# Optimization experiments

Hardware: AMD Instinct MI355X
Metric: run time of the kernel (lower is better)

Reference implementation:

```python
import math
import jax, jax.numpy as jnp
import numpy as np
from jax import lax

# FPN anchor layout: 1024x768 image, strides {4,8,16,32,64}, 3 anchors/location
NUM_PER_LEVEL = (147456, 36864, 9216, 2304, 576)
A_TOTAL = sum(NUM_PER_LEVEL)
BATCH = 8
PRE_NMS_TOP_N = 1000   # testing
POST_NMS_TOP_N = 1000  # testing
NMS_THRESH = 0.7
SCORE_THRESH = 0.0
MIN_SIZE = 1.0
IMG_H, IMG_W = 768.0, 1024.0
BBOX_XFORM_CLIP = math.log(1000.0 / 16.0)


def setup_inputs() -> dict:
    key = jax.random.key(0)
    k1, k2, k3, k4, k5, k6 = jax.random.split(key, 6)
    objectness = jax.random.normal(k1, (BATCH, A_TOTAL), jnp.float32)
    pred_bbox_deltas = jax.random.normal(k2, (BATCH, A_TOTAL, 4), jnp.float32) * 0.2
    # valid anchor boxes (x1, y1, x2, y2)
    cx = jax.random.uniform(k3, (A_TOTAL,), jnp.float32) * IMG_W
    cy = jax.random.uniform(k4, (A_TOTAL,), jnp.float32) * IMG_H
    w = 16.0 + jax.random.uniform(k5, (A_TOTAL,), jnp.float32) * 176.0
    h = 16.0 + jax.random.uniform(k6, (A_TOTAL,), jnp.float32) * 176.0
    anchors = jnp.stack([cx - 0.5 * w, cy - 0.5 * h, cx + 0.5 * w, cy + 0.5 * h], -1)
    return {"objectness": objectness, "pred_bbox_deltas": pred_bbox_deltas, "anchors": anchors}


def _nms_image(boxes, scores, lvl, valid):
    """batched_nms (level-offset trick) + post-NMS top-k, fixed shapes.
    boxes [K,4], scores [K], lvl [K] int, valid [K] bool -> [POST_NMS_TOP_N, 5]"""
    K = boxes.shape[0]
    s = jnp.where(valid, scores, -1.0)
    order = jnp.argsort(-s)  # decreasing score (invalid last)
    b = boxes[order]
    s = s[order]
    v = valid[order]
    # offset boxes per level so cross-level boxes never overlap (torchvision batched_nms)
    offset = lvl[order].astype(b.dtype) * (jnp.max(lax.stop_gradient(boxes)) + 1.0)
    nb = lax.stop_gradient(b) + offset[:, None]
    area = (nb[:, 2] - nb[:, 0]) * (nb[:, 3] - nb[:, 1])
    lt = jnp.maximum(nb[:, None, :2], nb[None, :, :2])  # [K,K,2]
    rb = jnp.minimum(nb[:, None, 2:], nb[None, :, 2:])
    wh = jnp.clip(rb - lt, 0.0)
    inter = wh[..., 0] * wh[..., 1]
    iou = inter / jnp.maximum(area[:, None] + area[None, :] - inter, 1e-9)
    pos = jnp.arange(K)

    def body(keep, i):
        sup = keep[i] & (iou[i] > NMS_THRESH) & (pos > i)
        return keep & ~sup, None

    keep, _ = lax.scan(body, v, pos)
    masked = jnp.where(keep, s, -1.0)
    top_s, top_i = lax.top_k(masked, POST_NMS_TOP_N)  # kept, decreasing score
    sel_b = b[top_i]
    ok = top_s > -0.5
    sel_b = jnp.where(ok[:, None], sel_b, 0.0)
    top_s = jnp.where(ok, top_s, 0.0)
    return jnp.concatenate([sel_b, top_s[:, None]], axis=-1)


def reference(objectness, pred_bbox_deltas, anchors):
    # --- box decode (BoxCoder, weights (1,1,1,1)) ---
    wa = anchors[:, 2] - anchors[:, 0]
    ha = anchors[:, 3] - anchors[:, 1]
    cxa = anchors[:, 0] + 0.5 * wa
    cya = anchors[:, 1] + 0.5 * ha
    dx, dy = pred_bbox_deltas[..., 0], pred_bbox_deltas[..., 1]
    dw = jnp.minimum(pred_bbox_deltas[..., 2], BBOX_XFORM_CLIP)
    dh = jnp.minimum(pred_bbox_deltas[..., 3], BBOX_XFORM_CLIP)
    pcx = dx * wa + cxa
    pcy = dy * ha + cya
    pw = jnp.exp(dw) * wa
    ph = jnp.exp(dh) * ha
    proposals = jnp.stack(
        [pcx - 0.5 * pw, pcy - 0.5 * ph, pcx + 0.5 * pw, pcy + 0.5 * ph], axis=-1
    )  # [B, A, 4]

    # --- per-level pre-NMS top-k (_get_top_n_idx) ---
    levels = jnp.concatenate(
        [jnp.full((n,), i, jnp.int32) for i, n in enumerate(NUM_PER_LEVEL)]
    )
    idx_parts = []
    off = 0
    for n in NUM_PER_LEVEL:
        k = min(PRE_NMS_TOP_N, n)
        _, ti = lax.top_k(objectness[:, off:off + n], k)
        idx_parts.append(ti + off)
        off += n
    top_idx = jnp.concatenate(idx_parts, axis=1)  # [B, K]

    scores = jax.nn.sigmoid(jnp.take_along_axis(objectness, top_idx, axis=1))
    lvl = levels[top_idx]
    boxes = jnp.take_along_axis(proposals, top_idx[..., None], axis=1)  # [B,K,4]

    # --- clip to image ---
    x1 = jnp.clip(boxes[..., 0], 0.0, IMG_W)
    y1 = jnp.clip(boxes[..., 1], 0.0, IMG_H)
    x2 = jnp.clip(boxes[..., 2], 0.0, IMG_W)
    y2 = jnp.clip(boxes[..., 3], 0.0, IMG_H)
    boxes = jnp.stack([x1, y1, x2, y2], axis=-1)

    # remove_small_boxes + score threshold (as validity mask; fixed shapes)
    valid = ((x2 - x1) >= MIN_SIZE) & ((y2 - y1) >= MIN_SIZE) & (scores >= SCORE_THRESH)

    # --- per-image batched NMS + post-NMS top-k ---
    return jax.vmap(_nms_image)(boxes, scores, lvl, valid)  # [B, POST_NMS_TOP_N, 5]
```

## Files before the change

kernel.cpp:

```cpp
#include <hip/hip_runtime.h>
#include <math.h>

#pragma clang fp contract(off)

#define A_TOTAL 196416
#define BATCH 8
#define KTOT 4576
#define NLEV 5
#define MSPLIT 16
#define RCAP 6144
#define NPARTS 48

static __device__ const int d_aoff[NLEV] = {0, 147456, 184320, 193536, 195840};
static __device__ const int d_n[NLEV]    = {147456, 36864, 9216, 2304, 576};
static __device__ const int d_k[NLEV]    = {1000, 1000, 1000, 1000, 576};
static __device__ const int d_spl[NLEV]  = {8, 2, 1, 1, 1};
static __device__ const int d_bp[NLEV]   = {0, 8, 10, 11, 12};
static __device__ const int d_pb_l[13]    = {0,0,0,0,0,0,0,0,1,1,2,3,4};
static __device__ const int d_pb_part[13] = {0,1,2,3,4,5,6,7,0,1,0,0,0};

#define TM_IOU (0.699999988079071044921875 + 0x1p-25)

__device__ inline unsigned int mono(float f) {
  unsigned int u = __float_as_uint(f);
  return (u & 0x80000000u) ? ~u : (u | 0x80000000u);
}
__device__ inline float imono(unsigned int m) {
  return __uint_as_float((m & 0x80000000u) ? (m & 0x7FFFFFFFu) : ~m);
}

__device__ inline int cnt_gt(const float* A, int n, float s) {
  int lo = 0, hi = n;
  while (lo < hi) { int mid = (lo + hi) >> 1; if (A[mid] > s) lo = mid + 1; else hi = mid; }
  return lo;
}
__device__ inline int cnt_ge(const float* A, int n, float s) {
  int lo = 0, hi = n;
  while (lo < hi) { int mid = (lo + hi) >> 1; if (A[mid] >= s) lo = mid + 1; else hi = mid; }
  return lo;
}

__global__ __launch_bounds__(1024) void k_hist(const float* __restrict__ obj,
                                               int* __restrict__ hist_g,
                                               int* __restrict__ cnt_g,
                                               float* __restrict__ maxblk) {
  int blk = blockIdx.x;
  int tid = threadIdx.x;
  if (blk == 0) {
    for (int i = tid; i < 40 * NPARTS; i += 1024) maxblk[i] = 0.0f;
    for (int i = tid; i < 40; i += 1024) cnt_g[i] = 0;
  }
  int b = blk / 13, pb = blk % 13;
  int l = d_pb_l[pb], part = d_pb_part[pb];
  int slice = d_n[l] / d_spl[l];
  int start = d_aoff[l] + part * slice;
  const float4* p4 = (const float4*)(obj + (size_t)b * A_TOTAL + start);
  int s4 = slice >> 2;
  __shared__ int h[4096];
  for (int i = tid; i < 4096; i += 1024) h[i] = 0;
  __syncthreads();
  for (int i = tid; i < s4; i += 1024) {
    float4 v = p4[i];
    atomicAdd(&h[mono(v.x) >> 20], 1);
    atomicAdd(&h[mono(v.y) >> 20], 1);
    atomicAdd(&h[mono(v.z) >> 20], 1);
    atomicAdd(&h[mono(v.w) >> 20], 1);
  }
  __syncthreads();
  int* outp = hist_g + (size_t)blk * 4096;
  for (int i = tid; i < 4096; i += 1024) outp[i] = h[i];
}

__global__ __launch_bounds__(1024) void k_collect(const float* __restrict__ obj,
                                                  const int* __restrict__ hist_g,
                                                  int* __restrict__ cnt_g,
                                                  unsigned long long* __restrict__ cand_g) {
  int blk = blockIdx.x;
  int b = blk / 13, pb = blk % 13;
  int l = d_pb_l[pb], part = d_pb_part[pb];
  int bl = b * NLEV + l;
  const int k = d_k[l];
  int tid = threadIdx.x, lane = tid & 63;
  __shared__ int t[4096];
  __shared__ int grp[256];
  __shared__ unsigned int sP;
  __shared__ __align__(16) unsigned long long lbuf[RCAP];
  __shared__ int s_cnt, s_base;
  int parts = d_spl[l];
  const int* hb = hist_g + (size_t)(b * 13 + d_bp[l]) * 4096;
  for (int bin = tid; bin < 4096; bin += 1024) {
    int s = 0;
    for (int p = 0; p < parts; ++p) s += hb[p * 4096 + bin];
    t[bin] = s;
  }
  if (tid == 0) s_cnt = 0;
  __syncthreads();
  if (tid < 256) {
    int s = 0;
    for (int j = 0; j < 16; ++j) s += t[tid * 16 + j];
    grp[tid] = s;
  }
  __syncthreads();
  if (tid == 0) {
    int cum = 0, g, d;
    for (g = 255; g >= 0; --g) {
      if (cum + grp[g] >= k) break;
      cum += grp[g];
    }
    for (d = 15; d >= 0; --d) {
      int c = t[g * 16 + d];
      if (cum + c >= k) break;
      cum += c;
    }
    sP = (unsigned int)(g * 16 + d);
  }
  __syncthreads();
  unsigned int P = sP;
  int slice = d_n[l] / parts;
  int start = d_aoff[l] + part * slice;
  const float4* p4 = (const float4*)(obj + (size_t)b * A_TOTAL + start);
  int s4 = slice >> 2;
  int lbase = part * slice;
  for (int i = tid; i < s4; i += 1024) {
    float4 v = p4[i];
    unsigned int a[4] = {mono(v.x), mono(v.y), mono(v.z), mono(v.w)};
#pragma unroll
    for (int c = 0; c < 4; ++c) {
      bool q = (a[c] >> 20) >= P;
      unsigned long long mb = __ballot(q);
      if (mb) {
        int base;
        if (lane == 0) base = atomicAdd(&s_cnt, __popcll(mb));
        base = __shfl(base, 0);
        if (q) {
          int slot = base + __popcll(mb & ((1ull << lane) - 1ull));
          if (slot < RCAP) {
            int idx = lbase + 4 * i + c;
            lbuf[slot] = ((unsigned long long)a[c] << 32) |
                         (unsigned int)(~(unsigned int)idx);
          }
        }
      }
    }
  }
  __syncthreads();
  int cnt = min(s_cnt, RCAP);
  if (tid == 0) s_base = atomicAdd(&cnt_g[bl], cnt);
  __syncthreads();
  int base = s_base;
  for (int i = tid; i < cnt; i += 1024) {
    int slot = base + i;
    if (slot < RCAP) cand_g[(size_t)bl * RCAP + slot] = lbuf[i];
  }
}

__device__ inline float decode_emit(unsigned long long e, int rank, int b,
                                    int k, int aoff, int bl,
                                    const float* __restrict__ deltas,
                                    const float* __restrict__ anchors,
                                    float* __restrict__ sc0,
                                    float4* __restrict__ box0) {
  if (rank >= k) return 0.0f;
  unsigned int k32 = (unsigned int)(e >> 32);
  unsigned int idx = ~(unsigned int)(e & 0xFFFFFFFFull);
  float o = imono(k32);
  int gidx = aoff + (int)idx;
  const float* dl = deltas + ((size_t)b * A_TOTAL + gidx) * 4;
  const float* an = anchors + (size_t)gidx * 4;
  float a0 = an[0], a1 = an[1], a2 = an[2], a3 = an[3];
  float wa = a2 - a0, ha = a3 - a1;
  float cxa = a0 + 0.5f * wa, cya = a1 + 0.5f * ha;
  float dx = dl[0], dy = dl[1];
  const float CLIPV = 4.135166556742356f;
  float dw = fminf(dl[2], CLIPV), dh = fminf(dl[3], CLIPV);
  float pcx = dx * wa + cxa;
  float pcy = dy * ha + cya;
  float pw = (float)exp((double)dw) * wa;
  float ph = (float)exp((double)dh) * ha;
  float x1 = pcx - 0.5f * pw, y1 = pcy - 0.5f * ph;
  float x2 = pcx + 0.5f * pw, y2 = pcy + 0.5f * ph;
  x1 = fminf(fmaxf(x1, 0.0f), 1024.0f);
  x2 = fminf(fmaxf(x2, 0.0f), 1024.0f);
  y1 = fminf(fmaxf(y1, 0.0f), 768.0f);
  y2 = fminf(fmaxf(y2, 0.0f), 768.0f);
  float s = (float)(1.0 / (1.0 + exp(-(double)o)));
  bool valid = ((x2 - x1) >= 1.0f) && ((y2 - y1) >= 1.0f) && (s >= 0.0f);
  sc0[bl * 1024 + rank] = valid ? s : -1.0f;
  box0[bl * 1024 + rank] = make_float4(x1, y1, x2, y2);
  return fmaxf(fmaxf(x1, y1), fmaxf(x2, y2));
}

__global__ __launch_bounds__(64) void k_rankdec(const unsigned long long* __restrict__ cand_g,
                                                const int* __restrict__ cnt_g,
                                                const float* __restrict__ deltas,
                                                const float* __restrict__ anchors,
                                                float* __restrict__ sc0,
                                                float4* __restrict__ box0,
                                                float* __restrict__ maxblk) {
  int bl = blockIdx.x / NPARTS, part = blockIdx.x % NPARTS;
  int b = bl / NLEV, l = bl % NLEV;
  const int k = d_k[l], aoff = d_aoff[l];
  int cnt = min(cnt_g[bl], RCAP);
  if (part * 128 >= cnt) return;
  __shared__ __align__(16) unsigned long long cb[RCAP];
  int tid = threadIdx.x;
  const unsigned long long* src = cand_g + (size_t)bl * RCAP;
  {
    const ulonglong2* s2 = (const ulonglong2*)src;
    ulonglong2* d2 = (ulonglong2*)cb;
    int n2 = cnt >> 1;
    for (int i = tid; i < n2; i += 64) d2[i] = s2[i];
    if ((cnt & 1) && tid == 0) cb[cnt - 1] = src[cnt - 1];
  }
  __syncthreads();
  int i0 = part * 128 + tid, i1 = i0 + 64;
  unsigned long long e0 = ~0ull, e1 = ~0ull;
  if (i0 < cnt) e0 = cb[i0];
  if (i1 < cnt) e1 = cb[i1];
  int r0 = 0, r1 = 0;
  int nc2 = cnt >> 1;
  const ulonglong2* c2 = (const ulonglong2*)cb;
  for (int j = 0; j < nc2; ++j) {
    ulonglong2 v = c2[j];
    r0 += (v.x > e0) + (v.y > e0);
    r1 += (v.x > e1) + (v.y > e1);
  }
  if (cnt & 1) {
    unsigned long long v = cb[cnt - 1];
    r0 += (v > e0);
    r1 += (v > e1);
  }
  float mx = 0.0f;
  if (i0 < cnt) mx = fmaxf(mx, decode_emit(e0, r0, b, k, aoff, bl, deltas, anchors, sc0, box0));
  if (i1 < cnt) mx = fmaxf(mx, decode_emit(e1, r1, b, k, aoff, bl, deltas, anchors, sc0, box0));
#pragma unroll
  for (int s = 1; s < 64; s <<= 1) mx = fmaxf(mx, __shfl_xor(mx, s));
  if (tid == 0) maxblk[blockIdx.x] = mx;
}

__global__ __launch_bounds__(1024) void k_mask(const float* __restrict__ sc0,
                                               const float4* __restrict__ box0,
                                               const float* __restrict__ maxblk,
                                               float* __restrict__ lvlsc,
                                               float4* __restrict__ lvlraw,
                                               int* __restrict__ g_V,
                                               unsigned long long* __restrict__ masks) {
  int blk = blockIdx.x;
  int bl = blk / MSPLIT, part = blk % MSPLIT;
  int b = bl / NLEV, l = bl % NLEV;
  const int k = d_k[l];
  int tid = threadIdx.x, lane = tid & 63, w = tid >> 6;
  __shared__ float4 lbox[1024];
  __shared__ float s_mv;
  __shared__ int s_wcnt[16];
  if (w == 0) {
    float v = 0.0f;
    for (int i = lane; i < NLEV * NPARTS; i += 64)
      v = fmaxf(v, maxblk[b * (NLEV * NPARTS) + i]);
#pragma unroll
    for (int s = 1; s < 64; s <<= 1) v = fmaxf(v, __shfl_xor(v, s));
    if (lane == 0) s_mv = v;
  }
  bool in = tid < k;
  float s = in ? sc0[bl * 1024 + tid] : -1.0f;
  bool valid = in && (s >= 0.0f);
  unsigned long long mb = __ballot(valid);
  if (lane == 0) s_wcnt[w] = __popcll(mb);
  __syncthreads();
  int pre = 0;
  for (int ww = 0; ww < w; ++ww) pre += s_wcnt[ww];
  int j = pre + __popcll(mb & ((1ull << lane) - 1ull));
  int V = 0;
  for (int ww = 0; ww < 16; ++ww) V += s_wcnt[ww];
  float off = (float)l * (s_mv + 1.0f);
  if (valid) {
    float4 bx = box0[bl * 1024 + tid];
    lbox[j] = make_float4(bx.x + off, bx.y + off, bx.z + off, bx.w + off);
    if (part == 0) {
      lvlsc[bl * 1024 + j] = s;
      lvlraw[bl * 1024 + j] = bx;
    }
  }
  if (part == 0 && tid == 0) g_V[bl] = V;
  __syncthreads();
  int row0 = part * 64;
  if (row0 >= V) return;
  int i = row0 + lane;
  if (i >= V) return;
  float4 bb = lbox[i];
  float ba = (bb.z - bb.x) * (bb.w - bb.y);
  unsigned long long bits = 0ull;
  int jbase = w * 64;
  if (jbase + 63 > i && jbase < V) {
    int jhi = min(64, V - jbase);
    for (int jo = 0; jo < jhi; ++jo) {
      int jj = jbase + jo;
      float4 cb = lbox[jj];
      float ca = (cb.z - cb.x) * (cb.w - cb.y);
      float xx1 = fmaxf(bb.x, cb.x), yy1 = fmaxf(bb.y, cb.y);
      float xx2 = fminf(bb.z, cb.z), yy2 = fminf(bb.w, cb.w);
      float wd = fmaxf(xx2 - xx1, 0.0f), ht = fmaxf(yy2 - yy1, 0.0f);
      float inter = wd * ht;
      float denom = fmaxf(ba + ca - inter, 1e-9f);
      if ((jj > i) && ((double)inter >= TM_IOU * (double)denom)) bits |= (1ull << jo);
    }
  }
  masks[((size_t)bl * 16 + w) * 1024 + i] = bits;
}

__global__ __launch_bounds__(1024) void k_scan(const unsigned long long* __restrict__ masks,
                                               const int* __restrict__ g_V,
                                               unsigned long long* __restrict__ keepbits) {
  int bl = blockIdx.x;
  int tid = threadIdx.x, lane = tid & 63, w = tid >> 6;
  int V = g_V[bl];
  const int nch = (V + 63) / 64;
  const unsigned long long* M = masks + (size_t)bl * 16 * 1024;
  __shared__ unsigned long long s_remv[16];
  __shared__ unsigned long long s_D[2][72];
  __shared__ unsigned long long s_dw;
  if (tid < 16) s_remv[tid] = ~0ull;
  int base_w = w * 64;
  unsigned long long init_w;
  if (V <= base_w) init_w = ~0ull;
  else if (V >= base_w + 64) init_w = 0ull;
  else init_w = (~0ull) << (V - base_w);
  if (w == 0 && nch > 0) s_D[0][lane] = (lane < V) ? M[lane] : 0ull;
  if (tid < 8) { s_D[0][64 + tid] = 0ull; s_D[1][64 + tid] = 0ull; }
  unsigned long long acc = 0ull;
  __syncthreads();

  for (int c = 0; c < nch; ++c) {
    unsigned long long val = 0ull;
    int r = 64 * c + lane;
    if (w > c && w < nch && r < V) val = M[(size_t)w * 1024 + r];
    if (w == c) {
      unsigned long long red = acc;
#pragma unroll
      for (int s = 1; s < 64; s <<= 1) red |= __shfl_xor(red, s);
      unsigned long long dw = init_w | red;
      const unsigned long long* D = s_D[c & 1];
      unsigned long long pb[8];
#pragma unroll
      for (int u = 0; u < 8; ++u) pb[u] = D[u];
#pragma unroll
      for (int g = 0; g < 8; ++g) {
#pragma unroll
        for (int u = 0; u < 8; ++u) {
          int jj = g * 8 + u;
          if (!((dw >> jj) & 1ull)) dw |= pb[u];
          pb[u] = D[jj + 8];
        }
      }
      if (lane == 0) { s_dw = dw; s_remv[c] = dw; }
    }
    if (w == c + 1 && w < nch) {
      int rr = 64 * (c + 1) + lane;
      s_D[(c + 1) & 1][lane] = (rr < V) ? M[(size_t)(c + 1) * 1024 + rr] : 0ull;
    }
    __syncthreads();
    if (w > c && w < nch) {
      unsigned long long kept = ~s_dw;
      if ((kept >> lane) & 1ull) acc |= val;
    }
    __syncthreads();
  }
  if (tid < 16) keepbits[bl * 16 + tid] = ~s_remv[tid];
}

__global__ __launch_bounds__(1024) void k_out(const float* __restrict__ lvlsc,
                                              const float4* __restrict__ lvlraw,
                                              const unsigned long long* __restrict__ keepbits,
                                              const int* __restrict__ g_V,
                                              float* __restrict__ out) {
  int b = blockIdx.x;
  int tid = threadIdx.x, lane = tid & 63, wv = tid >> 6;
  __shared__ float ksc[NLEV * 1024];
  __shared__ int kj[NLEV * 1024];
  __shared__ int sK[NLEV];
  __shared__ int s_wcnt[16];
  for (int i = tid; i < 5000; i += 1024) out[(size_t)b * 5000 + i] = 0.0f;
  for (int l = 0; l < NLEV; ++l) {
    int bl = b * NLEV + l;
    int V = g_V[bl];
    bool kept = (tid < V) && ((keepbits[bl * 16 + (tid >> 6)] >> (tid & 63)) & 1ull);
    unsigned long long mb = __ballot(kept);
    if (lane == 0) s_wcnt[wv] = __popcll(mb);
    __syncthreads();
    int pre = 0;
    for (int w = 0; w < wv; ++w) pre += s_wcnt[w];
    int r = pre + __popcll(mb & ((1ull << lane) - 1ull));
    if (kept) { ksc[l * 1024 + r] = lvlsc[bl * 1024 + tid]; kj[l * 1024 + r] = tid; }
    if (tid == 0) {
      int t = 0;
      for (int w = 0; w < 16; ++w) t += s_wcnt[w];
      sK[l] = t;
    }
    __syncthreads();
  }
  int K[NLEV];
  for (int l = 0; l < NLEV; ++l) K[l] = sK[l];
  for (int l = 0; l < NLEV; ++l) {
    if (tid < K[l]) {
      float s = ksc[l * 1024 + tid];
      int rank = tid;
      for (int l2 = 0; l2 < NLEV; ++l2) {
        if (l2 == l) continue;
        const float* A = ksc + l2 * 1024;
        rank += (l2 < l) ? cnt_ge(A, K[l2], s) : cnt_gt(A, K[l2], s);
      }
      if (rank < 1000) {
        float4 bx = lvlraw[(size_t)(b * NLEV + l) * 1024 + kj[l * 1024 + tid]];
        float* op = out + (size_t)b * 5000 + (size_t)rank * 5;
        op[0] = bx.x; op[1] = bx.y; op[2] = bx.z; op[3] = bx.w; op[4] = s;
      }
    }
  }
}

extern "C" void kernel_launch(void* const* d_in, const int* in_sizes, int n_in,
                              void* d_out, int out_size, void* d_ws, size_t ws_size,
                              hipStream_t stream) {
  const float* obj     = (const float*)d_in[0];
  const float* deltas  = (const float*)d_in[1];
  const float* anchors = (const float*)d_in[2];
  float* out = (float*)d_out;

  char* p = (char*)d_ws;
  float4* box0   = (float4*)p; p += (size_t)40 * 1024 * sizeof(float4);
  float4* lvlraw = (float4*)p; p += (size_t)40 * 1024 * sizeof(float4);
  unsigned long long* cand_g   = (unsigned long long*)p; p += (size_t)40 * RCAP * 8;
  unsigned long long* masks    = (unsigned long long*)p; p += (size_t)40 * 16 * 1024 * 8;
  unsigned long long* keepbits = (unsigned long long*)p; p += (size_t)40 * 16 * 8;
  int*   hist_g = (int*)p;   p += (size_t)104 * 4096 * 4;
  int*   cnt_g  = (int*)p;   p += 40 * 4;
  float* maxblk = (float*)p; p += (size_t)40 * NPARTS * 4;
  float* sc0    = (float*)p; p += (size_t)40 * 1024 * 4;
  float* lvlsc  = (float*)p; p += (size_t)40 * 1024 * 4;
  int*   g_V    = (int*)p;   p += 40 * 4;

  hipLaunchKernelGGL(k_hist, dim3(BATCH * 13), dim3(1024), 0, stream,
                     obj, hist_g, cnt_g, maxblk);
  hipLaunchKernelGGL(k_collect, dim3(BATCH * 13), dim3(1024), 0, stream,
                     obj, hist_g, cnt_g, cand_g);
  hipLaunchKernelGGL(k_rankdec, dim3(BATCH * NLEV * NPARTS), dim3(64), 0, stream,
                     cand_g, cnt_g, deltas, anchors, sc0, box0, maxblk);
  hipLaunchKernelGGL(k_mask, dim3(BATCH * NLEV * MSPLIT), dim3(1024), 0, stream,
                     sc0, box0, maxblk, lvlsc, lvlraw, g_V, masks);
  hipLaunchKernelGGL(k_scan, dim3(BATCH * NLEV), dim3(1024), 0, stream,
                     masks, g_V, keepbits);
  hipLaunchKernelGGL(k_out, dim3(BATCH), dim3(1024), 0, stream,
                     lvlsc, lvlraw, keepbits, g_V, out);
}
```

Before: 214.7 us.

## Fuse NMS scan with output merge and read rank candidates from global

Merges the per-level NMS scan kernel and the per-image output merge into one kernel. The level-0 block of each image spin-waits on an atomic done counter until all five level blocks have published their keep bits through atomicOr. This removes one kernel launch. In addition, k_rankdec no longer stages candidates in LDS and instead streams them from global memory with a 4-way unrolled compare loop, relying on cache hits. The spin-wait assumes all five level blocks of an image are co-resident, which holds for 40 blocks but adds a cross-block synchronisation dependency.

```diff
diff --git a/kernel.cpp b/kernel.cpp
--- a/kernel.cpp
+++ b/kernel.cpp
@@ -43,12 +43,16 @@
 __global__ __launch_bounds__(1024) void k_hist(const float* __restrict__ obj,
                                                int* __restrict__ hist_g,
                                                int* __restrict__ cnt_g,
-                                               float* __restrict__ maxblk) {
+                                               float* __restrict__ maxblk,
+                                               unsigned long long* __restrict__ keepbits,
+                                               int* __restrict__ done) {
   int blk = blockIdx.x;
   int tid = threadIdx.x;
   if (blk == 0) {
     for (int i = tid; i < 40 * NPARTS; i += 1024) maxblk[i] = 0.0f;
     for (int i = tid; i < 40; i += 1024) cnt_g[i] = 0;
+    for (int i = tid; i < 40 * 16; i += 1024) keepbits[i] = 0ull;
+    if (tid < BATCH) done[tid] = 0;
   }
   int b = blk / 13, pb = blk % 13;
   int l = d_pb_l[pb], part = d_pb_part[pb];
@@ -202,31 +206,30 @@
   const int k = d_k[l], aoff = d_aoff[l];
   int cnt = min(cnt_g[bl], RCAP);
   if (part * 128 >= cnt) return;
-  __shared__ __align__(16) unsigned long long cb[RCAP];
   int tid = threadIdx.x;
   const unsigned long long* src = cand_g + (size_t)bl * RCAP;
-  {
-    const ulonglong2* s2 = (const ulonglong2*)src;
-    ulonglong2* d2 = (ulonglong2*)cb;
-    int n2 = cnt >> 1;
-    for (int i = tid; i < n2; i += 64) d2[i] = s2[i];
-    if ((cnt & 1) && tid == 0) cb[cnt - 1] = src[cnt - 1];
-  }
-  __syncthreads();
   int i0 = part * 128 + tid, i1 = i0 + 64;
   unsigned long long e0 = ~0ull, e1 = ~0ull;
-  if (i0 < cnt) e0 = cb[i0];
-  if (i1 < cnt) e1 = cb[i1];
+  if (i0 < cnt) e0 = src[i0];
+  if (i1 < cnt) e1 = src[i1];
   int r0 = 0, r1 = 0;
+  const ulonglong2* c2 = (const ulonglong2*)src;
   int nc2 = cnt >> 1;
-  const ulonglong2* c2 = (const ulonglong2*)cb;
-  for (int j = 0; j < nc2; ++j) {
+  int j = 0;
+  for (; j + 4 <= nc2; j += 4) {
+    ulonglong2 v0 = c2[j], v1 = c2[j + 1], v2 = c2[j + 2], v3 = c2[j + 3];
+    r0 += (v0.x > e0) + (v0.y > e0) + (v1.x > e0) + (v1.y > e0) +
+          (v2.x > e0) + (v2.y > e0) + (v3.x > e0) + (v3.y > e0);
+    r1 += (v0.x > e1) + (v0.y > e1) + (v1.x > e1) + (v1.y > e1) +
+          (v2.x > e1) + (v2.y > e1) + (v3.x > e1) + (v3.y > e1);
+  }
+  for (; j < nc2; ++j) {
     ulonglong2 v = c2[j];
     r0 += (v.x > e0) + (v.y > e0);
     r1 += (v.x > e1) + (v.y > e1);
   }
   if (cnt & 1) {
-    unsigned long long v = cb[cnt - 1];
+    unsigned long long v = src[cnt - 1];
     r0 += (v > e0);
     r1 += (v > e1);
   }
@@ -308,10 +311,15 @@
   masks[((size_t)bl * 16 + w) * 1024 + i] = bits;
 }
 
-__global__ __launch_bounds__(1024) void k_scan(const unsigned long long* __restrict__ masks,
-                                               const int* __restrict__ g_V,
-                                               unsigned long long* __restrict__ keepbits) {
+__global__ __launch_bounds__(1024) void k_scanout(const unsigned long long* __restrict__ masks,
+                                                  const int* __restrict__ g_V,
+                                                  unsigned long long* __restrict__ keepbits,
+                                                  const float* __restrict__ lvlsc,
+                                                  const float4* __restrict__ lvlraw,
+                                                  int* __restrict__ done,
+                                                  float* __restrict__ out) {
   int bl = blockIdx.x;
+  int b = bl / NLEV, l = bl % NLEV;
   int tid = threadIdx.x, lane = tid & 63, w = tid >> 6;
   int V = g_V[bl];
   const int nch = (V + 63) / 64;
@@ -365,53 +373,61 @@
     }
     __syncthreads();
   }
-  if (tid < 16) keepbits[bl * 16 + tid] = ~s_remv[tid];
-}
-
-__global__ __launch_bounds__(1024) void k_out(const float* __restrict__ lvlsc,
-                                              const float4* __restrict__ lvlraw,
-                                              const unsigned long long* __restrict__ keepbits,
-                                              const int* __restrict__ g_V,
-                                              float* __restrict__ out) {
-  int b = blockIdx.x;
-  int tid = threadIdx.x, lane = tid & 63, wv = tid >> 6;
+  if (tid < 16) {
+    unsigned long long kb = ~s_remv[tid];
+    if (kb) atomicOr(&keepbits[bl * 16 + tid], kb);
+  }
+  __threadfence();
+  __syncthreads();
+  if (tid == 0) atomicAdd(&done[b], 1);
+  if (l != 0) return;
+
+  float* ob = out + (size_t)b * 5000;
+  for (int i = tid; i < 5000; i += 1024) ob[i] = 0.0f;
+  if (tid == 0) {
+    while (atomicAdd(&done[b], 0) < NLEV) __builtin_amdgcn_s_sleep(8);
+  }
+  __syncthreads();
+
   __shared__ float ksc[NLEV * 1024];
   __shared__ int kj[NLEV * 1024];
   __shared__ int sK[NLEV];
   __shared__ int s_wcnt[16];
-  for (int i = tid; i < 5000; i += 1024) out[(size_t)b * 5000 + i] = 0.0f;
-  for (int l = 0; l < NLEV; ++l) {
-    int bl = b * NLEV + l;
-    int V = g_V[bl];
-    bool kept = (tid < V) && ((keepbits[bl * 16 + (tid >> 6)] >> (tid & 63)) & 1ull);
+  for (int l2 = 0; l2 < NLEV; ++l2) {
+    int bl2 = b * NLEV + l2;
+    int V2 = g_V[bl2];
+    unsigned long long kbw = 0ull;
+    if (lane == 0) kbw = atomicAdd(&keepbits[bl2 * 16 + w], 0ull);
+    kbw = __shfl(kbw, 0);
+    bool kept = (tid < V2) && ((kbw >> lane) & 1ull);
     unsigned long long mb = __ballot(kept);
-    if (lane == 0) s_wcnt[wv] = __popcll(mb);
+    if (lane == 0) s_wcnt[w] = __popcll(mb);
     __syncthreads();
     int pre = 0;
-    for (int w = 0; w < wv; ++w) pre += s_wcnt[w];
+    for (int ww = 0; ww < w; ++ww) pre += s_wcnt[ww];
     int r = pre + __popcll(mb & ((1ull << lane) - 1ull));
-    if (kept) { ksc[l * 1024 + r] = lvlsc[bl * 1024 + tid]; kj[l * 1024 + r] = tid; }
+    if (kept) { ksc[l2 * 1024 + r] = lvlsc[bl2 * 1024 + tid]; kj[l2 * 1024 + r] = tid; }
     if (tid == 0) {
       int t = 0;
-      for (int w = 0; w < 16; ++w) t += s_wcnt[w];
-      sK[l] = t;
+      for (int ww = 0; ww < 16; ++ww) t += s_wcnt[ww];
+      sK[l2] = t;
     }
     __syncthreads();
   }
   int K[NLEV];
-  for (int l = 0; l < NLEV; ++l) K[l] = sK[l];
-  for (int l = 0; l < NLEV; ++l) {
-    if (tid < K[l]) {
-      float s = ksc[l * 1024 + tid];
+  for (int l2 = 0; l2 < NLEV; ++l2) K[l2] = sK[l2];
+  for (int l2 = 0; l2 < NLEV; ++l2) {
+    if (tid < K[l2]) {
+      float s = ksc[l2 * 1024 + tid];
       int rank = tid;
-      for (int l2 = 0; l2 < NLEV; ++l2) {
-        if (l2 == l) continue;
-        const float* A = ksc + l2 * 1024;
-        rank += (l2 < l) ? cnt_ge(A, K[l2], s) : cnt_gt(A, K[l2], s);
+      for (int l3 = 0; l3 < NLEV; ++l3) {
+        if (l3 == l2) continue;
+        const float* A = ksc + l3 * 1024;
+        rank += (l3 < l2) ? cnt_ge(A, K[l3], s) : cnt_gt(A, K[l3], s);
       }
       if (rank < 1000) {
-        float4 bx = lvlraw[(size_t)(b * NLEV + l) * 1024 + kj[l * 1024 + tid]];
-        float* op = out + (size_t)b * 5000 + (size_t)rank * 5;
+        float4 bx = lvlraw[(size_t)(b * NLEV + l2) * 1024 + kj[l2 * 1024 + tid]];
+        float* op = ob + (size_t)rank * 5;
         op[0] = bx.x; op[1] = bx.y; op[2] = bx.z; op[3] = bx.w; op[4] = s;
       }
     }
@@ -438,17 +454,16 @@
   float* sc0    = (float*)p; p += (size_t)40 * 1024 * 4;
   float* lvlsc  = (float*)p; p += (size_t)40 * 1024 * 4;
   int*   g_V    = (int*)p;   p += 40 * 4;
+  int*   done   = (int*)p;   p += BATCH * 4;
 
   hipLaunchKernelGGL(k_hist, dim3(BATCH * 13), dim3(1024), 0, stream,
-                     obj, hist_g, cnt_g, maxblk);
+                     obj, hist_g, cnt_g, maxblk, keepbits, done);
   hipLaunchKernelGGL(k_collect, dim3(BATCH * 13), dim3(1024), 0, stream,
                      obj, hist_g, cnt_g, cand_g);
   hipLaunchKernelGGL(k_rankdec, dim3(BATCH * NLEV * NPARTS), dim3(64), 0, stream,
                      cand_g, cnt_g, deltas, anchors, sc0, box0, maxblk);
   hipLaunchKernelGGL(k_mask, dim3(BATCH * NLEV * MSPLIT), dim3(1024), 0, stream,
                      sc0, box0, maxblk, lvlsc, lvlraw, g_V, masks);
-  hipLaunchKernelGGL(k_scan, dim3(BATCH * NLEV), dim3(1024), 0, stream,
-                     masks, g_V, keepbits);
-  hipLaunchKernelGGL(k_out, dim3(BATCH), dim3(1024), 0, stream,
-                     lvlsc, lvlraw, keepbits, g_V, out);
-}
+  hipLaunchKernelGGL(k_scanout, dim3(BATCH * NLEV), dim3(1024), 0, stream,
+                     masks, g_V, keepbits, lvlsc, lvlraw, done, out);
+}
```

New measurement: 262.3 us. +22.2%, slower.
